# Kernel tuning notes

Hardware: AMD Instinct MI355X
Metric: run time of the kernel (lower is better)

The kernel has to match this reference:

```python
import jax, jax.numpy as jnp
import numpy as np
from jax import lax

EPS = 1e-5
GROUPS = 8
TDVD_RANGE = 10
SCALE = 1.0
SCALE_FACTOR = 0.5


def setup_inputs() -> dict:
    key = jax.random.key(0)
    k1, k2 = jax.random.split(key)
    x = jax.random.normal(k1, (2, 16, 64, 128, 128), dtype=jnp.float32)
    gn_weight = jnp.ones((16,), dtype=jnp.float32)
    gn_bias = jnp.zeros((16,), dtype=jnp.float32)
    threshold = jnp.ones((1,), dtype=jnp.float32)  # torch fills with 1.0
    conv_weight = jax.random.normal(k2, (16, 16, 3, 3, 3), dtype=jnp.float32) * 0.05
    return {"x": x, "gn_weight": gn_weight, "gn_bias": gn_bias,
            "threshold": threshold, "conv_weight": conv_weight}


def _group_norm(x, w, b):
    B, C, D, H, W = x.shape
    xr = x.reshape(B, GROUPS, C // GROUPS, D, H, W)
    mean = xr.mean(axis=(2, 3, 4, 5), keepdims=True)
    var = xr.var(axis=(2, 3, 4, 5), keepdims=True)
    xn = ((xr - mean) * lax.rsqrt(var + EPS)).reshape(B, C, D, H, W)
    return xn * w.reshape(1, C, 1, 1, 1) + b.reshape(1, C, 1, 1, 1)


def _tdvd_histogram(x):
    # reverseint(x * scale * scale_factor) counted into 21 bins [-10..10], as %.
    y = x * (SCALE * SCALE_FACTOR)
    v = jnp.ceil(y * (y >= 0)) + jnp.floor(y * (y <= 0))
    idx = (v + TDVD_RANGE).astype(jnp.int32)
    valid = (idx >= 0) & (idx <= 2 * TDVD_RANGE)
    hist = jnp.zeros((2 * TDVD_RANGE + 1,), jnp.float32).at[
        jnp.clip(idx, 0, 2 * TDVD_RANGE)].add(jnp.where(valid, 1.0, 0.0))
    return hist / x.size * 100.0


def _threshold_func(x, threshold):
    thr = (threshold[0] + 0.0) / SCALE  # zero_point=0, scale=1.0
    t = jnp.transpose(x, (2, 0, 1, 3, 4))  # [D,B,C,H,W]
    front, back = t[:-1], t[1:]
    d = (back - front) / thr
    d = jnp.where(jnp.abs(d) > 1.0, d, 0.0)  # Hardshrink(1.0)
    d = d * lax.stop_gradient(thr)           # .item() detaches in torch
    out = jnp.concatenate([t[:1], front + d], axis=0)
    return jnp.transpose(out, (1, 2, 0, 3, 4))


def reference(x, gn_weight, gn_bias, threshold, conv_weight):
    x = jax.nn.relu(_group_norm(x, gn_weight, gn_bias))
    hist = _tdvd_histogram(x)
    x = _threshold_func(x, threshold)
    out = lax.conv_general_dilated(
        x, conv_weight, window_strides=(1, 1, 1),
        padding=((1, 1), (1, 1), (1, 1)),
        dimension_numbers=("NCDHW", "OIDHW", "NCDHW"))
    return out, hist
```

## Files before the change

### kernel.cpp

```cpp
#include <hip/hip_runtime.h>

typedef __attribute__((ext_vector_type(8))) short short8;
typedef __attribute__((ext_vector_type(4))) float f32x4;

#define GROUP_ELEMS 2097152
#define NBLK 64

__device__ inline short f2bf(float f) {
  unsigned u = __builtin_bit_cast(unsigned, f);
  unsigned r = (u + 0x7FFFu + ((u >> 16) & 1u)) >> 16;
  return (short)r;
}

__global__ __launch_bounds__(256) void k1_partials(const float* __restrict__ x,
                                                   float2* __restrict__ partials) {
  int group = blockIdx.x >> 6;
  int blk = blockIdx.x & 63;
  const float4* p = (const float4*)(x + (size_t)group * GROUP_ELEMS + (size_t)blk * 32768);
  float sum = 0.f, sq = 0.f;
  for (int i = threadIdx.x; i < 8192; i += 256) {
    float4 v = p[i];
    sum += v.x + v.y + v.z + v.w;
    sq  += v.x*v.x + v.y*v.y + v.z*v.z + v.w*v.w;
  }
  for (int off = 32; off; off >>= 1) {
    sum += __shfl_down(sum, off, 64);
    sq  += __shfl_down(sq,  off, 64);
  }
  __shared__ float2 sw[4];
  int lane = threadIdx.x & 63, wid = threadIdx.x >> 6;
  if (lane == 0) sw[wid] = make_float2(sum, sq);
  __syncthreads();
  if (threadIdx.x == 0) {
    float s = 0.f, q = 0.f;
    for (int j = 0; j < 4; ++j) { s += sw[j].x; q += sw[j].y; }
    partials[blockIdx.x] = make_float2(s, q);
  }
}

__global__ void k2_stats(const float2* __restrict__ partials,
                         float2* __restrict__ stats, int* __restrict__ hist) {
  int t = threadIdx.x;
  if (t < 16) {
    float s = 0.f, q = 0.f;
    for (int j = 0; j < NBLK; ++j) { float2 p = partials[t * NBLK + j]; s += p.x; q += p.y; }
    float mean = s / (float)GROUP_ELEMS;
    float var  = q / (float)GROUP_ELEMS - mean * mean;
    stats[t] = make_float2(mean, rsqrtf(var + 1e-5f));
  }
  if (t < 21) hist[t] = 0;
}

__global__ void k2b_wprep(const float* __restrict__ wgt, unsigned short* __restrict__ fbw) {
  int t = threadIdx.x;
  int cc = t >> 6, lane = t & 63;
  int m = lane & 15, g = lane >> 4;
  int icb = (g & 1) * 8, g2 = g >> 1;
  int kpos = 2 * cc + g2;
  short8 f;
  #pragma unroll
  for (int j = 0; j < 8; ++j)
    f[j] = (kpos <= 26) ? f2bf(wgt[m * 432 + (icb + j) * 27 + kpos]) : (short)0;
  *(short8*)(fbw + t * 8) = f;
}

__global__ __launch_bounds__(256) void k3_norm_thresh_hist(
    const float* __restrict__ x, const float* __restrict__ gw, const float* __restrict__ gb,
    const float* __restrict__ thrp, const float2* __restrict__ stats,
    unsigned short* __restrict__ z, int* __restrict__ hist) {
  __shared__ int sh[21];
  int t = threadIdx.x;
  if (t < 21) sh[t] = 0;
  __syncthreads();
  int hwl = t & 31, cp = t >> 5;
  int b = blockIdx.x >> 9;
  int hw = (blockIdx.x & 511) * 32 + hwl;
  int c0 = cp * 2, c1 = c0 + 1;
  float2 st = stats[b * 8 + cp];
  float A0 = gw[c0] * st.y, B0 = gb[c0] - st.x * A0;
  float A1 = gw[c1] * st.y, B1 = gb[c1] - st.x * A1;
  float thr = thrp[0];
  const float* px0 = x + (size_t)(b * 16 + c0) * 1048576 + hw;
  const float* px1 = x + (size_t)(b * 16 + c1) * 1048576 + hw;
  unsigned* pz = (unsigned*)(z + ((size_t)b * 64 * 16384 + hw) * 16 + c0);
  int c10 = 0, c11 = 0, c12 = 0;
  float xv0 = px0[0], xv1 = px1[0];
  float yp0 = 0.f, yp1 = 0.f;
  for (int d = 0; d < 64; ++d) {
    float n0 = 0.f, n1 = 0.f;
    if (d < 63) { n0 = px0[(d + 1) * 16384]; n1 = px1[(d + 1) * 16384]; }
    float y0 = fmaxf(fmaf(xv0, A0, B0), 0.f);
    float y1 = fmaxf(fmaf(xv1, A1, B1), 0.f);
    float v0 = ceilf(0.5f * y0);
    if (v0 == 0.f) c10++; else if (v0 == 1.f) c11++; else if (v0 == 2.f) c12++;
    else if (v0 <= 10.f) atomicAdd(&sh[(int)v0 + 10], 1);
    float v1 = ceilf(0.5f * y1);
    if (v1 == 0.f) c10++; else if (v1 == 1.f) c11++; else if (v1 == 2.f) c12++;
    else if (v1 <= 10.f) atomicAdd(&sh[(int)v1 + 10], 1);
    float z0, z1;
    if (d == 0) { z0 = y0; z1 = y1; }
    else {
      float dd0 = (y0 - yp0) / thr;
      z0 = (fabsf(dd0) > 1.f) ? fmaf(dd0, thr, yp0) : yp0;
      float dd1 = (y1 - yp1) / thr;
      z1 = (fabsf(dd1) > 1.f) ? fmaf(dd1, thr, yp1) : yp1;
    }
    unsigned u = (unsigned)(unsigned short)f2bf(z0) | ((unsigned)(unsigned short)f2bf(z1) << 16);
    pz[d * 131072] = u;
    yp0 = y0; yp1 = y1;
    xv0 = n0; xv1 = n1;
  }
  atomicAdd(&sh[10], c10);
  atomicAdd(&sh[11], c11);
  atomicAdd(&sh[12], c12);
  __syncthreads();
  if (t < 21) atomicAdd(&hist[t], sh[t]);
}

#define DT 8
#define PLANE 5440
__global__ __launch_bounds__(256, 4) void k4_conv(const unsigned short* __restrict__ z,
                                                  const unsigned short* __restrict__ fbw,
                                                  float* __restrict__ out) {
  __shared__ unsigned short lz[3 * PLANE];
  const int t = threadIdx.x;
  const int lane = t & 63, wid = t >> 6;
  const int b = blockIdx.z;
  const int d0 = blockIdx.y * DT;
  const int h0 = (blockIdx.x >> 2) * 8, w0 = (blockIdx.x & 3) * 32;
  const int m = lane & 15, g = lane >> 4;
  const int icb = (g & 1) * 8;
  const bool gs = (g >= 2);
  const int xw0 = ((m >> 2) & 1) << 3;
  const int xw1 = (((m + 1) >> 2) & 1) << 3;
  const int xw2 = (((m + 2) >> 2) & 1) << 3;

  short8 fb[14];
  #pragma unroll
  for (int cc = 0; cc < 14; ++cc)
    fb[cc] = *(const short8*)(fbw + (cc * 64 + lane) * 8);

  const unsigned short* zb = z + (size_t)b * 16777216;

  const int gi0 = t,        r0 = gi0 / 68, rm0 = gi0 - r0 * 68, s0 = rm0 >> 1, ig0 = rm0 & 1;
  const int gi1 = t + 256,  r1 = gi1 / 68, rm1 = gi1 - r1 * 68, s1 = rm1 >> 1, ig1 = rm1 & 1;
  const int gi2 = t + 512,  r2 = gi2 / 68, rm2 = gi2 - r2 * 68, s2 = rm2 >> 1, ig2 = rm2 & 1;
  const int hg0 = h0 - 1 + r0, wg0 = w0 - 1 + s0;
  const int hg1 = h0 - 1 + r1, wg1 = w0 - 1 + s1;
  const int hg2 = h0 - 1 + r2, wg2 = w0 - 1 + s2;
  const bool va0 = (unsigned)hg0 < 128u && (unsigned)wg0 < 128u;
  const bool va1 = (unsigned)hg1 < 128u && (unsigned)wg1 < 128u;
  const bool va2 = t < 168 && (unsigned)hg2 < 128u && (unsigned)wg2 < 128u;
  const int gof0 = (hg0 * 128 + wg0) * 16 + ig0 * 8;
  const int gof1 = (hg1 * 128 + wg1) * 16 + ig1 * 8;
  const int gof2 = (hg2 * 128 + wg2) * 16 + ig2 * 8;
  const int io0 = (r0 * 34 + s0) * 16 + (ig0 ^ ((s0 >> 2) & 1)) * 8;
  const int io1 = (r1 * 34 + s1) * 16 + (ig1 ^ ((s1 >> 2) & 1)) * 8;
  const int io2 = (r2 * 34 + s2) * 16 + (ig2 ^ ((s2 >> 2) & 1)) * 8;

  #pragma unroll
  for (int p = 0; p < 3; ++p) {
    const int dg = d0 - 1 + p;
    const bool dv = (unsigned)dg < 64u;
    short8 v0 = {0,0,0,0,0,0,0,0}, v1 = {0,0,0,0,0,0,0,0}, v2 = {0,0,0,0,0,0,0,0};
    if (dv && va0) v0 = *(const short8*)(zb + dg * 262144 + gof0);
    if (dv && va1) v1 = *(const short8*)(zb + dg * 262144 + gof1);
    if (dv && va2) v2 = *(const short8*)(zb + dg * 262144 + gof2);
    *(short8*)(&lz[p * PLANE + io0]) = v0;
    *(short8*)(&lz[p * PLANE + io1]) = v1;
    if (t < 168) *(short8*)(&lz[p * PLANE + io2]) = v2;
  }
  __syncthreads();

  int sA = 0, sB = PLANE, sC = 2 * PLANE;

  #pragma unroll 1
  for (int dl = 0; dl < DT; ++dl) {
    short8 sv0 = {0,0,0,0,0,0,0,0}, sv1 = {0,0,0,0,0,0,0,0}, sv2 = {0,0,0,0,0,0,0,0};
    const bool doStage = dl < DT - 1;
    if (doStage) {
      const int dg = d0 + dl + 2;
      const bool dv = (unsigned)dg < 64u;
      if (dv && va0) sv0 = *(const short8*)(zb + dg * 262144 + gof0);
      if (dv && va1) sv1 = *(const short8*)(zb + dg * 262144 + gof1);
      if (dv && va2) sv2 = *(const short8*)(zb + dg * 262144 + gof2);
    }
    #pragma unroll
    for (int q = 0; q < 4; ++q) {
      const int hl = wid * 2 + (q >> 1), wt = q & 1;
      const int qb = (hl * 34 + wt * 16 + m) * 16 + icb;
      f32x4 acc = {0.f, 0.f, 0.f, 0.f};
      __builtin_amdgcn_s_setprio(1);
      #pragma unroll
      for (int cc = 0; cc < 14; ++cc) {
        const int kp0 = 2 * cc;
        const int kp1 = (2 * cc + 1 > 26) ? 26 : 2 * cc + 1;
        const int kd0 = kp0 / 9, kh0 = (kp0 % 9) / 3, kw0 = kp0 % 3;
        const int kd1 = kp1 / 9, kh1 = (kp1 % 9) / 3, kw1 = kp1 % 3;
        const int co0 = (kh0 * 34 + kw0) * 16;
        const int co1 = (kh1 * 34 + kw1) * 16;
        const int ba0 = (kd0 == 0) ? sA : (kd0 == 1) ? sB : sC;
        const int ba1 = (kd1 == 0) ? sA : (kd1 == 1) ? sB : sC;
        const int xk0 = (kw0 == 0) ? xw0 : (kw0 == 1) ? xw1 : xw2;
        const int xk1 = (kw1 == 0) ? xw0 : (kw1 == 1) ? xw1 : xw2;
        const int off0 = (qb ^ xk0) + co0 + ba0;
        const int off1 = (qb ^ xk1) + co1 + ba1;
        const int off = gs ? off1 : off0;
        short8 a = *(const short8*)(&lz[off]);
        acc = __builtin_amdgcn_mfma_f32_16x16x32_bf16(a, fb[cc], acc, 0, 0, 0);
      }
      __builtin_amdgcn_s_setprio(0);
      float* op = out + (((size_t)(b * 16 + m) * 64 + (d0 + dl)) * 128 + (h0 + hl)) * 128
                  + w0 + wt * 16 + g * 4;
      *(float4*)op = make_float4(acc[0], acc[1], acc[2], acc[3]);
    }
    __syncthreads();
    if (doStage) {
      *(short8*)(&lz[sA + io0]) = sv0;
      *(short8*)(&lz[sA + io1]) = sv1;
      if (t < 168) *(short8*)(&lz[sA + io2]) = sv2;
      __syncthreads();
    }
    const int tmp = sA; sA = sB; sB = sC; sC = tmp;
  }
}

__global__ void k5_hist_out(const int* __restrict__ hist, float* __restrict__ out) {
  int t = threadIdx.x;
  if (t < 21) out[33554432u + t] = (float)hist[t] * (100.0f / 33554432.0f);
}

extern "C" void kernel_launch(void* const* d_in, const int* in_sizes, int n_in,
                              void* d_out, int out_size, void* d_ws, size_t ws_size,
                              hipStream_t stream) {
  (void)in_sizes; (void)n_in; (void)out_size; (void)ws_size;
  const float* x   = (const float*)d_in[0];
  const float* gw  = (const float*)d_in[1];
  const float* gb  = (const float*)d_in[2];
  const float* thr = (const float*)d_in[3];
  const float* cw  = (const float*)d_in[4];
  float* out = (float*)d_out;

  char* ws = (char*)d_ws;
  unsigned short* z = (unsigned short*)ws;
  float2* partials = (float2*)(ws + (size_t)67108864);
  float2* stats    = (float2*)(ws + (size_t)67108864 + 8192);
  int*    hist     = (int*)  (ws + (size_t)67108864 + 8192 + 128);
  unsigned short* fbw = (unsigned short*)(ws + (size_t)67108864 + 16384);

  k1_partials<<<1024, 256, 0, stream>>>(x, partials);
  k2_stats<<<1, 64, 0, stream>>>(partials, stats, hist);
  k2b_wprep<<<1, 896, 0, stream>>>(cw, fbw);
  k3_norm_thresh_hist<<<1024, 256, 0, stream>>>(x, gw, gb, thr, stats, z, hist);
  k4_conv<<<dim3(64, 8, 2), 256, 0, stream>>>(z, fbw, out);
  k5_hist_out<<<1, 64, 0, stream>>>(hist, out);
}
```

Before: 141.7 us.

## Vectorize norm/threshold pass, split depth into chunks, and fuse tiny launches

The normalize/threshold/histogram kernel now has each thread load float4 along W and covers a 16-deep depth chunk (with one halo plane recomputed), instead of scalar loads over all 64 depths. This gives wider loads and more independent blocks per column. The stats and weight-prep kernels are merged into one launch, and the histogram output is written by the first conv block, removing two launches. In exchange the halo plane is loaded twice, and each thread's bf16 stores are now strided by 8 words instead of contiguous.

```diff
diff --git a/kernel.cpp b/kernel.cpp
--- a/kernel.cpp
+++ b/kernel.cpp
@@ -38,8 +38,9 @@
   }
 }
 
-__global__ void k2_stats(const float2* __restrict__ partials,
-                         float2* __restrict__ stats, int* __restrict__ hist) {
+__global__ void k2_prep(const float2* __restrict__ partials, const float* __restrict__ wgt,
+                        float2* __restrict__ stats, int* __restrict__ hist,
+                        unsigned short* __restrict__ fbw) {
   int t = threadIdx.x;
   if (t < 16) {
     float s = 0.f, q = 0.f;
@@ -49,10 +50,6 @@
     stats[t] = make_float2(mean, rsqrtf(var + 1e-5f));
   }
   if (t < 21) hist[t] = 0;
-}
-
-__global__ void k2b_wprep(const float* __restrict__ wgt, unsigned short* __restrict__ fbw) {
-  int t = threadIdx.x;
   int cc = t >> 6, lane = t & 63;
   int m = lane & 15, g = lane >> 4;
   int icb = (g & 1) * 8, g2 = g >> 1;
@@ -72,42 +69,51 @@
   int t = threadIdx.x;
   if (t < 21) sh[t] = 0;
   __syncthreads();
-  int hwl = t & 31, cp = t >> 5;
-  int b = blockIdx.x >> 9;
-  int hw = (blockIdx.x & 511) * 32 + hwl;
+  int bx = blockIdx.x;
+  int b = bx >> 9, part = (bx >> 2) & 127, dchunk = bx & 3;
+  int cp = t >> 5, hwl = t & 31;
+  int hw = part * 128 + hwl * 4;
   int c0 = cp * 2, c1 = c0 + 1;
   float2 st = stats[b * 8 + cp];
   float A0 = gw[c0] * st.y, B0 = gb[c0] - st.x * A0;
   float A1 = gw[c1] * st.y, B1 = gb[c1] - st.x * A1;
   float thr = thrp[0];
-  const float* px0 = x + (size_t)(b * 16 + c0) * 1048576 + hw;
-  const float* px1 = x + (size_t)(b * 16 + c1) * 1048576 + hw;
-  unsigned* pz = (unsigned*)(z + ((size_t)b * 64 * 16384 + hw) * 16 + c0);
+  const f32x4* px0 = (const f32x4*)(x + (size_t)(b * 16 + c0) * 1048576 + hw);
+  const f32x4* px1 = (const f32x4*)(x + (size_t)(b * 16 + c1) * 1048576 + hw);
+  unsigned* pz = (unsigned*)(z + ((size_t)b * 1048576 + hw) * 16 + c0);
   int c10 = 0, c11 = 0, c12 = 0;
-  float xv0 = px0[0], xv1 = px1[0];
-  float yp0 = 0.f, yp1 = 0.f;
-  for (int d = 0; d < 64; ++d) {
-    float n0 = 0.f, n1 = 0.f;
-    if (d < 63) { n0 = px0[(d + 1) * 16384]; n1 = px1[(d + 1) * 16384]; }
-    float y0 = fmaxf(fmaf(xv0, A0, B0), 0.f);
-    float y1 = fmaxf(fmaf(xv1, A1, B1), 0.f);
-    float v0 = ceilf(0.5f * y0);
-    if (v0 == 0.f) c10++; else if (v0 == 1.f) c11++; else if (v0 == 2.f) c12++;
-    else if (v0 <= 10.f) atomicAdd(&sh[(int)v0 + 10], 1);
-    float v1 = ceilf(0.5f * y1);
-    if (v1 == 0.f) c10++; else if (v1 == 1.f) c11++; else if (v1 == 2.f) c12++;
-    else if (v1 <= 10.f) atomicAdd(&sh[(int)v1 + 10], 1);
-    float z0, z1;
-    if (d == 0) { z0 = y0; z1 = y1; }
-    else {
-      float dd0 = (y0 - yp0) / thr;
-      z0 = (fabsf(dd0) > 1.f) ? fmaf(dd0, thr, yp0) : yp0;
-      float dd1 = (y1 - yp1) / thr;
-      z1 = (fabsf(dd1) > 1.f) ? fmaf(dd1, thr, yp1) : yp1;
-    }
-    unsigned u = (unsigned)(unsigned short)f2bf(z0) | ((unsigned)(unsigned short)f2bf(z1) << 16);
-    pz[d * 131072] = u;
-    yp0 = y0; yp1 = y1;
+  const int lo = dchunk * 16, dend = lo + 16;
+  const int dstart = (lo == 0) ? 0 : lo - 1;
+  f32x4 xv0 = px0[(size_t)dstart * 4096], xv1 = px1[(size_t)dstart * 4096];
+  float yp0[4], yp1[4];
+  for (int d = dstart; d < dend; ++d) {
+    f32x4 n0 = {0.f,0.f,0.f,0.f}, n1 = {0.f,0.f,0.f,0.f};
+    if (d + 1 < dend) { n0 = px0[(size_t)(d + 1) * 4096]; n1 = px1[(size_t)(d + 1) * 4096]; }
+    bool act = (d >= lo);
+    #pragma unroll
+    for (int k = 0; k < 4; ++k) {
+      float y0 = fmaxf(fmaf(xv0[k], A0, B0), 0.f);
+      float y1 = fmaxf(fmaf(xv1[k], A1, B1), 0.f);
+      if (act) {
+        float v0 = ceilf(0.5f * y0);
+        if (v0 == 0.f) c10++; else if (v0 == 1.f) c11++; else if (v0 == 2.f) c12++;
+        else if (v0 <= 10.f) atomicAdd(&sh[(int)v0 + 10], 1);
+        float v1 = ceilf(0.5f * y1);
+        if (v1 == 0.f) c10++; else if (v1 == 1.f) c11++; else if (v1 == 2.f) c12++;
+        else if (v1 <= 10.f) atomicAdd(&sh[(int)v1 + 10], 1);
+        float z0, z1;
+        if (d == 0) { z0 = y0; z1 = y1; }
+        else {
+          float dd0 = (y0 - yp0[k]) / thr;
+          z0 = (fabsf(dd0) > 1.f) ? fmaf(dd0, thr, yp0[k]) : yp0[k];
+          float dd1 = (y1 - yp1[k]) / thr;
+          z1 = (fabsf(dd1) > 1.f) ? fmaf(dd1, thr, yp1[k]) : yp1[k];
+        }
+        unsigned u = (unsigned)(unsigned short)f2bf(z0) | ((unsigned)(unsigned short)f2bf(z1) << 16);
+        pz[d * 131072 + k * 8] = u;
+      }
+      yp0[k] = y0; yp1[k] = y1;
+    }
     xv0 = n0; xv1 = n1;
   }
   atomicAdd(&sh[10], c10);
@@ -121,9 +127,12 @@
 #define PLANE 5440
 __global__ __launch_bounds__(256, 4) void k4_conv(const unsigned short* __restrict__ z,
                                                   const unsigned short* __restrict__ fbw,
+                                                  const int* __restrict__ hist,
                                                   float* __restrict__ out) {
   __shared__ unsigned short lz[3 * PLANE];
   const int t = threadIdx.x;
+  if (blockIdx.x == 0 && blockIdx.y == 0 && blockIdx.z == 0 && t < 21)
+    out[33554432u + t] = (float)hist[t] * (100.0f / 33554432.0f);
   const int lane = t & 63, wid = t >> 6;
   const int b = blockIdx.z;
   const int d0 = blockIdx.y * DT;
@@ -225,11 +234,6 @@
   }
 }
 
-__global__ void k5_hist_out(const int* __restrict__ hist, float* __restrict__ out) {
-  int t = threadIdx.x;
-  if (t < 21) out[33554432u + t] = (float)hist[t] * (100.0f / 33554432.0f);
-}
-
 extern "C" void kernel_launch(void* const* d_in, const int* in_sizes, int n_in,
                               void* d_out, int out_size, void* d_ws, size_t ws_size,
                               hipStream_t stream) {
@@ -243,15 +247,13 @@
 
   char* ws = (char*)d_ws;
   unsigned short* z = (unsigned short*)ws;
-  float2* partials = (float2*)(ws + (size_t)67108864);
-  float2* stats    = (float2*)(ws + (size_t)67108864 + 8192);
-  int*    hist     = (int*)  (ws + (size_t)67108864 + 8192 + 128);
+  float2* partials  = (float2*)(ws + (size_t)67108864);
+  float2* stats     = (float2*)(ws + (size_t)67108864 + 8192);
+  int*    hist      = (int*)  (ws + (size_t)67108864 + 8192 + 128);
   unsigned short* fbw = (unsigned short*)(ws + (size_t)67108864 + 16384);
 
   k1_partials<<<1024, 256, 0, stream>>>(x, partials);
-  k2_stats<<<1, 64, 0, stream>>>(partials, stats, hist);
-  k2b_wprep<<<1, 896, 0, stream>>>(cw, fbw);
+  k2_prep<<<1, 896, 0, stream>>>(partials, cw, stats, hist, fbw);
   k3_norm_thresh_hist<<<1024, 256, 0, stream>>>(x, gw, gb, thr, stats, z, hist);
-  k4_conv<<<dim3(64, 8, 2), 256, 0, stream>>>(z, fbw, out);
-  k5_hist_out<<<1, 64, 0, stream>>>(hist, out);
-}
+  k4_conv<<<dim3(64, 8, 2), 256, 0, stream>>>(z, fbw, hist, out);
+}
```

After: 151.1 us. +6.7%, slower.
